# Kernel optimization log

Hardware: AMD Instinct MI355X
Metric: run time of the kernel (lower is better)

The kernel has to match this reference:

```python
import jax, jax.numpy as jnp
import numpy as np

BATCH, T, D_MODEL, D_STATE = 32, 4096, 256, 256
RMIN, RMAX, MAX_PHASE = 0.9, 0.999, 6.283
NEG_SLOPE = 0.01  # F.leaky_relu default


def setup_inputs() -> dict:
    key = jax.random.key(0)
    ks = jax.random.split(key, 12)
    x = jax.random.normal(ks[0], (BATCH, T, D_MODEL), jnp.float32)
    done = jnp.zeros((BATCH, T), jnp.bool_)
    h0_re = jnp.zeros((BATCH, D_STATE), jnp.float32)
    h0_im = jnp.zeros((BATCH, D_STATE), jnp.float32)
    # LRU eigenvalue init: |lambda| ~ U[rmin, rmax] (Orvieto et al.)
    u1 = jax.random.uniform(ks[1], (D_STATE,), jnp.float32)
    u2 = jax.random.uniform(ks[2], (D_STATE,), jnp.float32)
    nu_log = jnp.log(-0.5 * jnp.log(u1 * (RMAX**2 - RMIN**2) + RMIN**2))
    theta_log = jnp.log(MAX_PHASE * u2)
    lam_abs = jnp.exp(-jnp.exp(nu_log))
    gamma_log = jnp.log(jnp.sqrt(1.0 - lam_abs**2))
    sB = 1.0 / np.sqrt(2.0 * D_MODEL)
    sC = 1.0 / np.sqrt(D_STATE)
    B_re = jax.random.normal(ks[3], (D_STATE, D_MODEL), jnp.float32) * sB
    B_im = jax.random.normal(ks[4], (D_STATE, D_MODEL), jnp.float32) * sB
    C_re = jax.random.normal(ks[5], (D_STATE, D_STATE), jnp.float32) * sC
    C_im = jax.random.normal(ks[6], (D_STATE, D_STATE), jnp.float32) * sC
    D_mat = jax.random.normal(ks[7], (D_STATE, D_MODEL), jnp.float32) * (1.0 / np.sqrt(D_MODEL))
    mlp_w = jax.random.normal(ks[8], (D_MODEL, D_STATE), jnp.float32) * (1.0 / np.sqrt(D_STATE))
    mlp_b = jnp.zeros((D_MODEL,), jnp.float32)
    ln1_g = jnp.ones((D_MODEL,), jnp.float32); ln1_b = jnp.zeros((D_MODEL,), jnp.float32)
    ln2_g = jnp.ones((D_STATE,), jnp.float32); ln2_b = jnp.zeros((D_STATE,), jnp.float32)
    ln3_g = jnp.ones((D_MODEL,), jnp.float32); ln3_b = jnp.zeros((D_MODEL,), jnp.float32)
    return dict(x=x, done=done, h0_re=h0_re, h0_im=h0_im, nu_log=nu_log,
                theta_log=theta_log, gamma_log=gamma_log, B_re=B_re, B_im=B_im,
                C_re=C_re, C_im=C_im, D_mat=D_mat, mlp_w=mlp_w, mlp_b=mlp_b,
                ln1_g=ln1_g, ln1_b=ln1_b, ln2_g=ln2_g, ln2_b=ln2_b,
                ln3_g=ln3_g, ln3_b=ln3_b)


def _layernorm(x, g, b, eps=1e-5):
    mu = jnp.mean(x, axis=-1, keepdims=True)
    var = jnp.var(x, axis=-1, keepdims=True)
    return (x - mu) * jax.lax.rsqrt(var + eps) * g + b


def _leaky(x):
    return jnp.where(x >= 0, x, NEG_SLOPE * x)


def _forward(x, done, h0_re, h0_im, nu_log, theta_log, gamma_log, B_re, B_im,
             C_re, C_im, D_mat, mlp_w, mlp_b, ln1_g, ln1_b, ln2_g, ln2_b,
             ln3_g, ln3_b):
    z = _layernorm(x, ln1_g, ln1_b)          # [B,T,D]
    skip = z
    z = _leaky(z)
    # diagonal complex recurrence params
    lam_abs = jnp.exp(-jnp.exp(nu_log))
    theta = jnp.exp(theta_log)
    lam_re = lam_abs * jnp.cos(theta)        # [N]
    lam_im = lam_abs * jnp.sin(theta)
    gamma = jnp.exp(gamma_log)
    # input projection: gamma * (B z_t), complex
    u_re = jnp.einsum('btd,nd->btn', z, B_re) * gamma
    u_im = jnp.einsum('btd,nd->btn', z, B_im) * gamma
    mask = 1.0 - done.astype(z.dtype)        # [B,T], reset state where done

    def step(carry, inp):
        hr, hi = carry
        ur, ui, m = inp                       # [B,N],[B,N],[B]
        hr = hr * m[:, None]
        hi = hi * m[:, None]
        nr = lam_re * hr - lam_im * hi + ur
        ni = lam_re * hi + lam_im * hr + ui
        return (nr, ni), (nr, ni)

    xs = (jnp.swapaxes(u_re, 0, 1), jnp.swapaxes(u_im, 0, 1), jnp.swapaxes(mask, 0, 1))
    (_, _), (hs_re, hs_im) = jax.lax.scan(step, (h0_re, h0_im), xs)
    hs_re = jnp.swapaxes(hs_re, 0, 1)         # [B,T,N]
    hs_im = jnp.swapaxes(hs_im, 0, 1)
    # y = Re(C h) + D z
    y = (jnp.einsum('btn,mn->btm', hs_re, C_re)
         - jnp.einsum('btn,mn->btm', hs_im, C_im)
         + jnp.einsum('btd,nd->btn', z, D_mat))
    y = _leaky(_layernorm(y, ln2_g, ln2_b))
    y = jnp.einsum('btn,dn->btd', y, mlp_w) + mlp_b
    y = _layernorm(y, ln3_g, ln3_b)
    return y + skip


def reference(x, done, h0_re, h0_im, nu_log, theta_log, gamma_log, B_re, B_im,
              C_re, C_im, D_mat, mlp_w, mlp_b, ln1_g, ln1_b, ln2_g, ln2_b,
              ln3_g, ln3_b):
    return _forward(x, done, h0_re, h0_im, nu_log, theta_log, gamma_log,
                    B_re, B_im, C_re, C_im, D_mat, mlp_w, mlp_b,
                    ln1_g, ln1_b, ln2_g, ln2_b, ln3_g, ln3_b)
```

## Files before the change

kernel.cpp:

```cpp
#include <hip/hip_runtime.h>

#define BATCH 32
#define TLEN  4096
#define DM    256
#define NS    256
#define BT    (BATCH*TLEN)
#define CHL   64
#define NCH   (TLEN/CHL)

typedef unsigned short u16;
typedef __bf16 bf16x8 __attribute__((ext_vector_type(8)));
typedef float  f32x4  __attribute__((ext_vector_type(4)));

__device__ __forceinline__ u16 f2bf(float f) {
  unsigned u = __builtin_bit_cast(unsigned, f);
  u += 0x7FFFu + ((u >> 16) & 1u);
  return (u16)(u >> 16);
}
__device__ __forceinline__ float bf2f(u16 h) {
  unsigned u = ((unsigned)h) << 16;
  return __builtin_bit_cast(float, u);
}
__device__ __forceinline__ float wsum(float v) {
  #pragma unroll
  for (int m = 32; m >= 1; m >>= 1) v += __shfl_xor(v, m, 64);
  return v;
}
__device__ __forceinline__ void gload_lds16(const void* g, void* l) {
  __builtin_amdgcn_global_load_lds(
      (const __attribute__((address_space(1))) void*)(uintptr_t)g,
      (__attribute__((address_space(3))) void*)(unsigned)(uintptr_t)l,
      16, 0, 0);
}
#define VMCNT(N)  asm volatile("s_waitcnt vmcnt(" #N ")" ::: "memory")
#define LGKM0()   asm volatile("s_waitcnt lgkmcnt(0)" ::: "memory")
#define BARRIER() do { __builtin_amdgcn_s_barrier(); asm volatile("" ::: "memory"); } while (0)

__global__ void k_prep(const float* __restrict__ nu_log, const float* __restrict__ th_log,
                       const float* __restrict__ ga_log,
                       const float* __restrict__ B_re, const float* __restrict__ B_im,
                       const float* __restrict__ C_re, const float* __restrict__ C_im,
                       const float* __restrict__ D_mat, const float* __restrict__ mlp_w,
                       float* __restrict__ lam_re, float* __restrict__ lam_im,
                       u16* __restrict__ WB, u16* __restrict__ W2, u16* __restrict__ WM)
{
  const int tid = blockIdx.x * blockDim.x + threadIdx.x;
  const int nt  = gridDim.x * blockDim.x;
  for (int i = tid; i < NS; i += nt) {
    float la = expf(-expf(nu_log[i]));
    float th = expf(th_log[i]);
    lam_re[i] = la * cosf(th);
    lam_im[i] = la * sinf(th);
  }
  for (int i = tid; i < 512 * DM; i += nt) {
    int n = i >> 8, d = i & 255;
    float v = (n < 256) ? B_re[n * DM + d] * expf(ga_log[n])
                        : B_im[(n - 256) * DM + d] * expf(ga_log[n - 256]);
    WB[i] = f2bf(v);
  }
  for (int i = tid; i < 256 * 768; i += nt) {
    int n = i / 768, k = i - n * 768;
    float v;
    if (k < 256)      v =  C_re[n * 256 + k];
    else if (k < 512) v = -C_im[n * 256 + (k - 256)];
    else              v =  D_mat[n * 256 + (k - 512)];
    W2[i] = f2bf(v);
  }
  for (int i = tid; i < 256 * 256; i += nt) WM[i] = f2bf(mlp_w[i]);
}

__global__ __launch_bounds__(256) void k_ln1(const float* __restrict__ x,
                                             const float* __restrict__ g, const float* __restrict__ b,
                                             u16* __restrict__ zskip, u16* __restrict__ za)
{
  const size_t row = (size_t)blockIdx.x * 4 + (threadIdx.x >> 6);
  const int lane = threadIdx.x & 63;
  float4 v = ((const float4*)(x + row * DM))[lane];
  float s = wsum(v.x + v.y + v.z + v.w);
  float q = wsum(v.x * v.x + v.y * v.y + v.z * v.z + v.w * v.w);
  float mean = s * (1.f / DM);
  float rstd = rsqrtf(q * (1.f / DM) - mean * mean + 1e-5f);
  float4 gg = ((const float4*)g)[lane];
  float4 bb = ((const float4*)b)[lane];
  float z0 = (v.x - mean) * rstd * gg.x + bb.x;
  float z1 = (v.y - mean) * rstd * gg.y + bb.y;
  float z2 = (v.z - mean) * rstd * gg.z + bb.z;
  float z3 = (v.w - mean) * rstd * gg.w + bb.w;
  ushort4 zs, zl;
  zs.x = f2bf(z0); zs.y = f2bf(z1); zs.z = f2bf(z2); zs.w = f2bf(z3);
  zl.x = f2bf(z0 >= 0.f ? z0 : 0.01f * z0);
  zl.y = f2bf(z1 >= 0.f ? z1 : 0.01f * z1);
  zl.z = f2bf(z2 >= 0.f ? z2 : 0.01f * z2);
  zl.w = f2bf(z3 >= 0.f ? z3 : 0.01f * z3);
  ((ushort4*)(zskip + row * DM))[lane] = zs;
  ((ushort4*)(za    + row * DM))[lane] = zl;
}

template <int EPI>
__global__ __launch_bounds__(512, 2) void gemm_fused(
    const u16* __restrict__ A0, int lda0, int ksplit,
    const u16* __restrict__ A1, int lda1,
    int K, const u16* __restrict__ W, int ldw,
    const float* __restrict__ g, const float* __restrict__ b,
    const float* __restrict__ bias, const u16* __restrict__ zskip,
    u16* __restrict__ outb, float* __restrict__ outf, int ldo)
{
  __shared__ __align__(16) u16 As[2][256 * 64];
  __shared__ __align__(16) u16 Bs[2][256 * 64];
  const int m0 = blockIdx.x * 256;
  const int nw0 = blockIdx.y << 8;
  const int tid = threadIdx.x;
  const int w = tid >> 6, lane = tid & 63;
  const int wr = w >> 1, wc = w & 1;

  f32x4 acc[4][8] = {};

  auto STAGE_A = [&](int p, int k0, int half) {
    const bool second = (k0 >= ksplit);
    const u16* Asrc = second ? A1 : A0;
    const int  alda = second ? lda1 : lda0;
    const int  ak   = second ? (k0 - ksplit) : k0;
    #pragma unroll
    for (int j = 0; j < 2; ++j) {
      const int r = half * 16 + w * 2 + j;
      const int row = r * 8 + (lane >> 3);
      const int col = (((lane & 7) ^ (row & 7)) << 3);
      gload_lds16(Asrc + (size_t)(m0 + row) * alda + ak + col, &As[p][r * 512]);
    }
  };
  auto STAGE_B = [&](int p, int k0, int half) {
    #pragma unroll
    for (int j = 0; j < 2; ++j) {
      const int r = half * 16 + w * 2 + j;
      const int row = r * 8 + (lane >> 3);
      const int col = (((lane & 7) ^ (row & 7)) << 3);
      gload_lds16(W + (size_t)(nw0 + row) * ldw + k0 + col, &Bs[p][r * 512]);
    }
  };

  const int NT = K >> 6;
  STAGE_A(0, 0, 0); STAGE_A(0, 0, 1);
  STAGE_B(0, 0, 0); STAGE_B(0, 0, 1);
  if (NT > 1) { STAGE_A(1, 64, 0); STAGE_A(1, 64, 1); VMCNT(4); }
  else        { VMCNT(0); }
  BARRIER();

  const int lq = (lane >> 4) << 3;

  for (int t = 0; t < NT; ++t) {
    const int p = t & 1;
    const int pn = p ^ 1;
    bf16x8 af[4][2];
    bf16x8 bfr[2][2];

    #pragma unroll
    for (int mi = 0; mi < 4; ++mi) {
      const int ra = wr * 64 + mi * 16 + (lane & 15);
      #pragma unroll
      for (int kki = 0; kki < 2; ++kki) {
        const int koff = kki * 32 + lq;
        af[mi][kki] = *(const bf16x8*)((const char*)&As[p][0] + ra * 128 + ((koff * 2) ^ ((ra & 7) << 4)));
      }
    }
    #pragma unroll
    for (int nn = 0; nn < 2; ++nn) {
      const int rb = wc * 128 + nn * 16 + (lane & 15);
      #pragma unroll
      for (int kki = 0; kki < 2; ++kki) {
        const int koff = kki * 32 + lq;
        bfr[nn][kki] = *(const bf16x8*)((const char*)&Bs[p][0] + rb * 128 + ((koff * 2) ^ ((rb & 7) << 4)));
      }
    }
    if (t + 1 < NT) STAGE_B(pn, (t + 1) << 6, 0);
    BARRIER(); LGKM0();
    __builtin_amdgcn_s_setprio(1);
    #pragma unroll
    for (int kki = 0; kki < 2; ++kki)
      #pragma unroll
      for (int nn = 0; nn < 2; ++nn)
        #pragma unroll
        for (int mi = 0; mi < 4; ++mi)
          acc[mi][nn] = __builtin_amdgcn_mfma_f32_16x16x32_bf16(af[mi][kki], bfr[nn][kki], acc[mi][nn], 0, 0, 0);
    __builtin_amdgcn_s_setprio(0);
    BARRIER();

    #pragma unroll
    for (int q = 1; q < 4; ++q) {
      #pragma unroll
      for (int nn = 0; nn < 2; ++nn) {
        const int rb = wc * 128 + (q * 2 + nn) * 16 + (lane & 15);
        #pragma unroll
        for (int kki = 0; kki < 2; ++kki) {
          const int koff = kki * 32 + lq;
          bfr[nn][kki] = *(const bf16x8*)((const char*)&Bs[p][0] + rb * 128 + ((koff * 2) ^ ((rb & 7) << 4)));
        }
      }
      if (q == 1)      { if (t + 1 < NT) STAGE_B(pn, (t + 1) << 6, 1); }
      else if (q == 2) { if (t + 2 < NT) STAGE_A(p,  (t + 2) << 6, 0); }
      else             { if (t + 2 < NT) STAGE_A(p,  (t + 2) << 6, 1); }
      BARRIER(); LGKM0();
      __builtin_amdgcn_s_setprio(1);
      #pragma unroll
      for (int kki = 0; kki < 2; ++kki)
        #pragma unroll
        for (int nn = 0; nn < 2; ++nn)
          #pragma unroll
          for (int mi = 0; mi < 4; ++mi)
            acc[mi][q * 2 + nn] = __builtin_amdgcn_mfma_f32_16x16x32_bf16(af[mi][kki], bfr[nn][kki], acc[mi][q * 2 + nn], 0, 0, 0);
      __builtin_amdgcn_s_setprio(0);
      if (q == 3) { if (t + 2 < NT) { VMCNT(4); } else { VMCNT(0); } }
      BARRIER();
    }
  }

  const int rq = (lane >> 4) << 2;

  if constexpr (EPI == 0) {
    #pragma unroll
    for (int mi = 0; mi < 4; ++mi) {
      #pragma unroll
      for (int rr = 0; rr < 4; ++rr) {
        const int row = wr * 64 + mi * 16 + rq + rr;
        const size_t rbase = (size_t)(m0 + row) * ldo + nw0;
        #pragma unroll
        for (int ni = 0; ni < 8; ++ni) {
          const int col = wc * 128 + ni * 16 + (lane & 15);
          outb[rbase + col] = f2bf(acc[mi][ni][rr]);
        }
      }
    }
    return;
  }

  float g8[8], b8[8], bias8[8];
  #pragma unroll
  for (int ni = 0; ni < 8; ++ni) {
    const int col = wc * 128 + ni * 16 + (lane & 15);
    g8[ni] = g[col]; b8[ni] = b[col];
    if constexpr (EPI == 2) bias8[ni] = bias[col];
  }

  float* red = (float*)&As[0][0];
  #pragma unroll
  for (int mi = 0; mi < 4; ++mi) {
    #pragma unroll
    for (int rr = 0; rr < 4; ++rr) {
      float s = 0.f, q = 0.f;
      #pragma unroll
      for (int ni = 0; ni < 8; ++ni) {
        float v = acc[mi][ni][rr];
        if constexpr (EPI == 2) v += bias8[ni];
        s += v; q += v * v;
      }
      #pragma unroll
      for (int mm = 1; mm < 16; mm <<= 1) {
        s += __shfl_xor(s, mm, 64);
        q += __shfl_xor(q, mm, 64);
      }
      if ((lane & 15) == 0) {
        const int row = wr * 64 + mi * 16 + rq + rr;
        red[row * 4 + wc * 2]     = s;
        red[row * 4 + wc * 2 + 1] = q;
      }
    }
  }
  __syncthreads();

  #pragma unroll
  for (int mi = 0; mi < 4; ++mi) {
    #pragma unroll
    for (int rr = 0; rr < 4; ++rr) {
      const int row = wr * 64 + mi * 16 + rq + rr;
      const float S = red[row * 4] + red[row * 4 + 2];
      const float Q = red[row * 4 + 1] + red[row * 4 + 3];
      const float mean = S * (1.f / 256.f);
      const float rstd = rsqrtf(Q * (1.f / 256.f) - mean * mean + 1e-5f);
      const size_t rbase = (size_t)(m0 + row) * 256;
      #pragma unroll
      for (int ni = 0; ni < 8; ++ni) {
        const int col = wc * 128 + ni * 16 + (lane & 15);
        float v = acc[mi][ni][rr];
        if constexpr (EPI == 2) v += bias8[ni];
        float t = (v - mean) * rstd * g8[ni] + b8[ni];
        if constexpr (EPI == 1) {
          t = t >= 0.f ? t : 0.01f * t;
          outb[rbase + col] = f2bf(t);
        } else {
          outf[rbase + col] = t + bf2f(zskip[rbase + col]);
        }
      }
    }
  }
}

__global__ __launch_bounds__(256) void scan_passA(const u16* __restrict__ u,
    const unsigned char* __restrict__ done,
    const float* __restrict__ lam_re, const float* __restrict__ lam_im,
    float* __restrict__ Ere, float* __restrict__ Eim,
    float* __restrict__ Are, float* __restrict__ Aim)
{
  const int b = blockIdx.x / NCH, c = blockIdx.x % NCH;
  const int n = threadIdx.x;
  const float lr = lam_re[n], li = lam_im[n];
  float hre = 0.f, him = 0.f, pm = 1.f;
  const int t0 = c * CHL;
  for (int t = t0; t < t0 + CHL; ++t) {
    const float m = done[b * TLEN + t] ? 0.f : 1.f;
    pm *= m;
    const float hr = hre * m, hi = him * m;
    const size_t base = ((size_t)(b * TLEN + t)) * 512;
    const float ur = bf2f(u[base + n]), ui = bf2f(u[base + 256 + n]);
    hre = lr * hr - li * hi + ur;
    him = lr * hi + li * hr + ui;
  }
  const size_t idx = ((size_t)(b * NCH + c)) * NS + n;
  Ere[idx] = hre; Eim[idx] = him;
  float pr = lr, pi = li;
  #pragma unroll
  for (int s = 0; s < 6; ++s) { float a = pr * pr - pi * pi; float bq = 2.f * pr * pi; pr = a; pi = bq; }
  Are[idx] = pr * pm; Aim[idx] = pi * pm;
}

__global__ __launch_bounds__(256) void scan_comb(const float* __restrict__ h0re,
    const float* __restrict__ h0im,
    const float* __restrict__ Are, const float* __restrict__ Aim,
    const float* __restrict__ Ere, const float* __restrict__ Eim,
    float* __restrict__ Sre, float* __restrict__ Sim)
{
  const int b = blockIdx.x, n = threadIdx.x;
  float sre = h0re[b * NS + n], sim = h0im[b * NS + n];
  for (int c = 0; c < NCH; ++c) {
    const size_t idx = ((size_t)(b * NCH + c)) * NS + n;
    Sre[idx] = sre; Sim[idx] = sim;
    const float ar = Are[idx], ai = Aim[idx];
    const float nr = ar * sre - ai * sim + Ere[idx];
    const float ni = ar * sim + ai * sre + Eim[idx];
    sre = nr; sim = ni;
  }
}

__global__ __launch_bounds__(256) void scan_passC(u16* __restrict__ u,
    const unsigned char* __restrict__ done,
    const float* __restrict__ lam_re, const float* __restrict__ lam_im,
    const float* __restrict__ Sre, const float* __restrict__ Sim)
{
  const int b = blockIdx.x / NCH, c = blockIdx.x % NCH;
  const int n = threadIdx.x;
  const float lr = lam_re[n], li = lam_im[n];
  const size_t sidx = ((size_t)(b * NCH + c)) * NS + n;
  float hre = Sre[sidx], him = Sim[sidx];
  const int t0 = c * CHL;
  for (int t = t0; t < t0 + CHL; ++t) {
    const float m = done[b * TLEN + t] ? 0.f : 1.f;
    const float hr = hre * m, hi = him * m;
    const size_t base = ((size_t)(b * TLEN + t)) * 512;
    const float ur = bf2f(u[base + n]), ui = bf2f(u[base + 256 + n]);
    hre = lr * hr - li * hi + ur;
    him = lr * hi + li * hr + ui;
    u[base + n]       = f2bf(hre);
    u[base + 256 + n] = f2bf(him);
  }
}

extern "C" void kernel_launch(void* const* d_in, const int* in_sizes, int n_in,
                              void* d_out, int out_size, void* d_ws, size_t ws_size,
                              hipStream_t stream)
{
  const float* x      = (const float*)d_in[0];
  const unsigned char* done = (const unsigned char*)d_in[1];
  const float* h0re   = (const float*)d_in[2];
  const float* h0im   = (const float*)d_in[3];
  const float* nu_log = (const float*)d_in[4];
  const float* th_log = (const float*)d_in[5];
  const float* ga_log = (const float*)d_in[6];
  const float* B_re   = (const float*)d_in[7];
  const float* B_im   = (const float*)d_in[8];
  const float* C_re   = (const float*)d_in[9];
  const float* C_im   = (const float*)d_in[10];
  const float* D_mat  = (const float*)d_in[11];
  const float* mlp_w  = (const float*)d_in[12];
  const float* mlp_b  = (const float*)d_in[13];
  const float* ln1_g  = (const float*)d_in[14];
  const float* ln1_b  = (const float*)d_in[15];
  const float* ln2_g  = (const float*)d_in[16];
  const float* ln2_b  = (const float*)d_in[17];
  const float* ln3_g  = (const float*)d_in[18];
  const float* ln3_b  = (const float*)d_in[19];
  (void)in_sizes; (void)n_in; (void)out_size; (void)ws_size;

  char* ws = (char*)d_ws;
  float* lam_re = (float*)(ws + 0);
  float* lam_im = (float*)(ws + 1024);
  u16* WB = (u16*)(ws + 4096);
  u16* W2 = (u16*)(ws + 4096 + 512 * 256 * 2);
  u16* WM = (u16*)(ws + 4096 + 512 * 256 * 2 + 256 * 768 * 2);

  size_t off = (size_t)1 << 20;
  u16* zskip = (u16*)(ws + off); off += (size_t)BT * DM * 2;
  u16* za    = (u16*)(ws + off); off += (size_t)BT * DM * 2;
  u16* ubuf  = (u16*)(ws + off); off += (size_t)BT * 512 * 2;
  u16* ybuf  = (u16*)(ws + off); off += (size_t)BT * NS * 2;
  float* Ere = (float*)(ws + off); off += (size_t)BATCH * NCH * NS * 4;
  float* Eim = (float*)(ws + off); off += (size_t)BATCH * NCH * NS * 4;
  float* Are = (float*)(ws + off); off += (size_t)BATCH * NCH * NS * 4;
  float* Aim = (float*)(ws + off); off += (size_t)BATCH * NCH * NS * 4;
  float* Sre = (float*)(ws + off); off += (size_t)BATCH * NCH * NS * 4;
  float* Sim = (float*)(ws + off); off += (size_t)BATCH * NCH * NS * 4;

  k_prep<<<256, 256, 0, stream>>>(nu_log, th_log, ga_log, B_re, B_im, C_re, C_im,
                                  D_mat, mlp_w, lam_re, lam_im, WB, W2, WM);
  k_ln1<<<BT / 4, 256, 0, stream>>>(x, ln1_g, ln1_b, zskip, za);
  gemm_fused<0><<<dim3(BT / 256, 2), 512, 0, stream>>>(za, 256, 1 << 28, nullptr, 0,
                                                       256, WB, 256, nullptr, nullptr,
                                                       nullptr, nullptr, ubuf, nullptr, 512);
  scan_passA<<<BATCH * NCH, 256, 0, stream>>>(ubuf, done, lam_re, lam_im, Ere, Eim, Are, Aim);
  scan_comb <<<BATCH,       256, 0, stream>>>(h0re, h0im, Are, Aim, Ere, Eim, Sre, Sim);
  scan_passC<<<BATCH * NCH, 256, 0, stream>>>(ubuf, done, lam_re, lam_im, Sre, Sim);
  gemm_fused<1><<<dim3(BT / 256, 1), 512, 0, stream>>>(ubuf, 512, 512, za, 256,
                                                       768, W2, 768, ln2_g, ln2_b,
                                                       nullptr, nullptr, ybuf, nullptr, 256);
  gemm_fused<2><<<dim3(BT / 256, 1), 512, 0, stream>>>(ybuf, 256, 256, ybuf, 256,
                                                       256, WM, 256, ln3_g, ln3_b,
                                                       mlp_b, zskip, nullptr, (float*)d_out, 256);
}
```

Measured before the change: 349.6 us.

## Fuse LN2 GEMM and MLP GEMM with LN3 into one megakernel

Merges the second GEMM (with LN2+leaky epilogue) and the MLP GEMM (with LN3 and skip add) into a single kernel. The intermediate activation stays in shared memory as bf16 instead of being written to and re-read from a global ybuf. The first GEMM is also specialized with compile-time K and strides. The second GEMM reads the MLP weights straight from global memory without LDS staging, which may stall on memory latency, and the extra accumulator registers may hurt occupancy.

```diff
diff --git a/kernel.cpp b/kernel.cpp
--- a/kernel.cpp
+++ b/kernel.cpp
@@ -96,14 +96,9 @@
   ((ushort4*)(za    + row * DM))[lane] = zl;
 }
 
-template <int EPI>
-__global__ __launch_bounds__(512, 2) void gemm_fused(
-    const u16* __restrict__ A0, int lda0, int ksplit,
-    const u16* __restrict__ A1, int lda1,
-    int K, const u16* __restrict__ W, int ldw,
-    const float* __restrict__ g, const float* __restrict__ b,
-    const float* __restrict__ bias, const u16* __restrict__ zskip,
-    u16* __restrict__ outb, float* __restrict__ outf, int ldo)
+__global__ __launch_bounds__(512, 2) void gemm_u4(
+    const u16* __restrict__ A0, const u16* __restrict__ W,
+    u16* __restrict__ outb)
 {
   __shared__ __align__(16) u16 As[2][256 * 64];
   __shared__ __align__(16) u16 Bs[2][256 * 64];
@@ -116,16 +111,12 @@
   f32x4 acc[4][8] = {};
 
   auto STAGE_A = [&](int p, int k0, int half) {
-    const bool second = (k0 >= ksplit);
-    const u16* Asrc = second ? A1 : A0;
-    const int  alda = second ? lda1 : lda0;
-    const int  ak   = second ? (k0 - ksplit) : k0;
     #pragma unroll
     for (int j = 0; j < 2; ++j) {
       const int r = half * 16 + w * 2 + j;
       const int row = r * 8 + (lane >> 3);
       const int col = (((lane & 7) ^ (row & 7)) << 3);
-      gload_lds16(Asrc + (size_t)(m0 + row) * alda + ak + col, &As[p][r * 512]);
+      gload_lds16(A0 + (size_t)(m0 + row) * 256 + k0 + col, &As[p][r * 512]);
     }
   };
   auto STAGE_B = [&](int p, int k0, int half) {
@@ -134,15 +125,14 @@
       const int r = half * 16 + w * 2 + j;
       const int row = r * 8 + (lane >> 3);
       const int col = (((lane & 7) ^ (row & 7)) << 3);
-      gload_lds16(W + (size_t)(nw0 + row) * ldw + k0 + col, &Bs[p][r * 512]);
+      gload_lds16(W + (size_t)(nw0 + row) * 256 + k0 + col, &Bs[p][r * 512]);
     }
   };
 
-  const int NT = K >> 6;
+  const int NT = 4;
   STAGE_A(0, 0, 0); STAGE_A(0, 0, 1);
   STAGE_B(0, 0, 0); STAGE_B(0, 0, 1);
-  if (NT > 1) { STAGE_A(1, 64, 0); STAGE_A(1, 64, 1); VMCNT(4); }
-  else        { VMCNT(0); }
+  STAGE_A(1, 64, 0); STAGE_A(1, 64, 1); VMCNT(4);
   BARRIER();
 
   const int lq = (lane >> 4) << 3;
@@ -214,44 +204,152 @@
   }
 
   const int rq = (lane >> 4) << 2;
-
-  if constexpr (EPI == 0) {
+  #pragma unroll
+  for (int mi = 0; mi < 4; ++mi) {
+    #pragma unroll
+    for (int rr = 0; rr < 4; ++rr) {
+      const int row = wr * 64 + mi * 16 + rq + rr;
+      const size_t rbase = (size_t)(m0 + row) * 512 + nw0;
+      #pragma unroll
+      for (int ni = 0; ni < 8; ++ni) {
+        const int col = wc * 128 + ni * 16 + (lane & 15);
+        outb[rbase + col] = f2bf(acc[mi][ni][rr]);
+      }
+    }
+  }
+}
+
+__global__ __launch_bounds__(512, 2) void gemm_mega(
+    const u16* __restrict__ A0, int lda0, int ksplit,
+    const u16* __restrict__ A1, int lda1,
+    int K, const u16* __restrict__ W, int ldw,
+    const float* __restrict__ g2, const float* __restrict__ b2,
+    const u16* __restrict__ WM, const float* __restrict__ mlp_b,
+    const float* __restrict__ g3, const float* __restrict__ b3,
+    const u16* __restrict__ zskip, float* __restrict__ outf)
+{
+  __shared__ __align__(16) u16 SH[4 * 256 * 64];
+  const int m0 = blockIdx.x * 256;
+  const int tid = threadIdx.x;
+  const int w = tid >> 6, lane = tid & 63;
+  const int wr = w >> 1, wc = w & 1;
+
+  f32x4 acc[4][8] = {};
+
+  auto STAGE_A = [&](int p, int k0, int half) {
+    const bool second = (k0 >= ksplit);
+    const u16* Asrc = second ? A1 : A0;
+    const int  alda = second ? lda1 : lda0;
+    const int  ak   = second ? (k0 - ksplit) : k0;
+    #pragma unroll
+    for (int j = 0; j < 2; ++j) {
+      const int r = half * 16 + w * 2 + j;
+      const int row = r * 8 + (lane >> 3);
+      const int col = (((lane & 7) ^ (row & 7)) << 3);
+      gload_lds16(Asrc + (size_t)(m0 + row) * alda + ak + col, SH + p * 16384 + r * 512);
+    }
+  };
+  auto STAGE_B = [&](int p, int k0, int half) {
+    #pragma unroll
+    for (int j = 0; j < 2; ++j) {
+      const int r = half * 16 + w * 2 + j;
+      const int row = r * 8 + (lane >> 3);
+      const int col = (((lane & 7) ^ (row & 7)) << 3);
+      gload_lds16(W + (size_t)row * ldw + k0 + col, SH + 32768 + p * 16384 + r * 512);
+    }
+  };
+
+  const int NT = K >> 6;
+  STAGE_A(0, 0, 0); STAGE_A(0, 0, 1);
+  STAGE_B(0, 0, 0); STAGE_B(0, 0, 1);
+  STAGE_A(1, 64, 0); STAGE_A(1, 64, 1); VMCNT(4);
+  BARRIER();
+
+  const int lq = (lane >> 4) << 3;
+
+  for (int t = 0; t < NT; ++t) {
+    const int p = t & 1;
+    const int pn = p ^ 1;
+    const u16* Ab = SH + p * 16384;
+    const u16* Bb = SH + 32768 + p * 16384;
+    bf16x8 af[4][2];
+    bf16x8 bfr[2][2];
+
     #pragma unroll
     for (int mi = 0; mi < 4; ++mi) {
-      #pragma unroll
-      for (int rr = 0; rr < 4; ++rr) {
-        const int row = wr * 64 + mi * 16 + rq + rr;
-        const size_t rbase = (size_t)(m0 + row) * ldo + nw0;
+      const int ra = wr * 64 + mi * 16 + (lane & 15);
+      #pragma unroll
+      for (int kki = 0; kki < 2; ++kki) {
+        const int koff = kki * 32 + lq;
+        af[mi][kki] = *(const bf16x8*)((const char*)Ab + ra * 128 + ((koff * 2) ^ ((ra & 7) << 4)));
+      }
+    }
+    #pragma unroll
+    for (int nn = 0; nn < 2; ++nn) {
+      const int rb = wc * 128 + nn * 16 + (lane & 15);
+      #pragma unroll
+      for (int kki = 0; kki < 2; ++kki) {
+        const int koff = kki * 32 + lq;
+        bfr[nn][kki] = *(const bf16x8*)((const char*)Bb + rb * 128 + ((koff * 2) ^ ((rb & 7) << 4)));
+      }
+    }
+    if (t + 1 < NT) STAGE_B(pn, (t + 1) << 6, 0);
+    BARRIER(); LGKM0();
+    __builtin_amdgcn_s_setprio(1);
+    #pragma unroll
+    for (int kki = 0; kki < 2; ++kki)
+      #pragma unroll
+      for (int nn = 0; nn < 2; ++nn)
         #pragma unroll
-        for (int ni = 0; ni < 8; ++ni) {
-          const int col = wc * 128 + ni * 16 + (lane & 15);
-          outb[rbase + col] = f2bf(acc[mi][ni][rr]);
+        for (int mi = 0; mi < 4; ++mi)
+          acc[mi][nn] = __builtin_amdgcn_mfma_f32_16x16x32_bf16(af[mi][kki], bfr[nn][kki], acc[mi][nn], 0, 0, 0);
+    __builtin_amdgcn_s_setprio(0);
+    BARRIER();
+
+    #pragma unroll
+    for (int q = 1; q < 4; ++q) {
+      #pragma unroll
+      for (int nn = 0; nn < 2; ++nn) {
+        const int rb = wc * 128 + (q * 2 + nn) * 16 + (lane & 15);
+        #pragma unroll
+        for (int kki = 0; kki < 2; ++kki) {
+          const int koff = kki * 32 + lq;
+          bfr[nn][kki] = *(const bf16x8*)((const char*)Bb + rb * 128 + ((koff * 2) ^ ((rb & 7) << 4)));
         }
       }
-    }
-    return;
-  }
-
-  float g8[8], b8[8], bias8[8];
+      if (q == 1)      { if (t + 1 < NT) STAGE_B(pn, (t + 1) << 6, 1); }
+      else if (q == 2) { if (t + 2 < NT) STAGE_A(p,  (t + 2) << 6, 0); }
+      else             { if (t + 2 < NT) STAGE_A(p,  (t + 2) << 6, 1); }
+      BARRIER(); LGKM0();
+      __builtin_amdgcn_s_setprio(1);
+      #pragma unroll
+      for (int kki = 0; kki < 2; ++kki)
+        #pragma unroll
+        for (int nn = 0; nn < 2; ++nn)
+          #pragma unroll
+          for (int mi = 0; mi < 4; ++mi)
+            acc[mi][q * 2 + nn] = __builtin_amdgcn_mfma_f32_16x16x32_bf16(af[mi][kki], bfr[nn][kki], acc[mi][q * 2 + nn], 0, 0, 0);
+      __builtin_amdgcn_s_setprio(0);
+      if (q == 3) { if (t + 2 < NT) { VMCNT(4); } else { VMCNT(0); } }
+      BARRIER();
+    }
+  }
+
+  const int rq = (lane >> 4) << 2;
+  float g8[8], b8[8];
   #pragma unroll
   for (int ni = 0; ni < 8; ++ni) {
     const int col = wc * 128 + ni * 16 + (lane & 15);
-    g8[ni] = g[col]; b8[ni] = b[col];
-    if constexpr (EPI == 2) bias8[ni] = bias[col];
-  }
-
-  float* red = (float*)&As[0][0];
+    g8[ni] = g2[col]; b8[ni] = b2[col];
+  }
+  float* red = (float*)SH;
   #pragma unroll
   for (int mi = 0; mi < 4; ++mi) {
     #pragma unroll
     for (int rr = 0; rr < 4; ++rr) {
       float s = 0.f, q = 0.f;
       #pragma unroll
-      for (int ni = 0; ni < 8; ++ni) {
-        float v = acc[mi][ni][rr];
-        if constexpr (EPI == 2) v += bias8[ni];
-        s += v; q += v * v;
-      }
+      for (int ni = 0; ni < 8; ++ni) { float v = acc[mi][ni][rr]; s += v; q += v * v; }
       #pragma unroll
       for (int mm = 1; mm < 16; mm <<= 1) {
         s += __shfl_xor(s, mm, 64);
@@ -265,29 +363,102 @@
     }
   }
   __syncthreads();
-
+  float mean2[4][4], rstd2[4][4];
   #pragma unroll
   for (int mi = 0; mi < 4; ++mi) {
     #pragma unroll
     for (int rr = 0; rr < 4; ++rr) {
       const int row = wr * 64 + mi * 16 + rq + rr;
-      const float S = red[row * 4] + red[row * 4 + 2];
-      const float Q = red[row * 4 + 1] + red[row * 4 + 3];
+      const f32x4 rv = *(const f32x4*)(red + row * 4);
+      const float S = rv[0] + rv[2], Q = rv[1] + rv[3];
+      mean2[mi][rr] = S * (1.f / 256.f);
+      rstd2[mi][rr] = rsqrtf(Q * (1.f / 256.f) - mean2[mi][rr] * mean2[mi][rr] + 1e-5f);
+    }
+  }
+  __syncthreads();
+  #pragma unroll
+  for (int mi = 0; mi < 4; ++mi) {
+    #pragma unroll
+    for (int rr = 0; rr < 4; ++rr) {
+      const int row = wr * 64 + mi * 16 + rq + rr;
+      #pragma unroll
+      for (int ni = 0; ni < 8; ++ni) {
+        const int col = wc * 128 + ni * 16 + (lane & 15);
+        float t = (acc[mi][ni][rr] - mean2[mi][rr]) * rstd2[mi][rr] * g8[ni] + b8[ni];
+        t = t >= 0.f ? t : 0.01f * t;
+        SH[row * 256 + (col ^ ((row & 7) << 3))] = f2bf(t);
+      }
+    }
+  }
+  __syncthreads();
+
+  f32x4 acc2[4][8] = {};
+  #pragma unroll
+  for (int s = 0; s < 8; ++s) {
+    const int k = s * 32 + lq;
+    bf16x8 af2[4], bf2[8];
+    #pragma unroll
+    for (int mi = 0; mi < 4; ++mi) {
+      const int row = wr * 64 + mi * 16 + (lane & 15);
+      af2[mi] = *(const bf16x8*)&SH[row * 256 + (k ^ ((row & 7) << 3))];
+    }
+    #pragma unroll
+    for (int ni = 0; ni < 8; ++ni) {
+      const int col = wc * 128 + ni * 16 + (lane & 15);
+      bf2[ni] = *(const bf16x8*)(WM + (size_t)col * 256 + k);
+    }
+    #pragma unroll
+    for (int ni = 0; ni < 8; ++ni)
+      #pragma unroll
+      for (int mi = 0; mi < 4; ++mi)
+        acc2[mi][ni] = __builtin_amdgcn_mfma_f32_16x16x32_bf16(af2[mi], bf2[ni], acc2[mi][ni], 0, 0, 0);
+  }
+  __syncthreads();
+
+  float bias8[8], g38[8], b38[8];
+  #pragma unroll
+  for (int ni = 0; ni < 8; ++ni) {
+    const int col = wc * 128 + ni * 16 + (lane & 15);
+    bias8[ni] = mlp_b[col]; g38[ni] = g3[col]; b38[ni] = b3[col];
+  }
+  #pragma unroll
+  for (int mi = 0; mi < 4; ++mi) {
+    #pragma unroll
+    for (int rr = 0; rr < 4; ++rr) {
+      float s = 0.f, q = 0.f;
+      #pragma unroll
+      for (int ni = 0; ni < 8; ++ni) {
+        float v = acc2[mi][ni][rr] + bias8[ni];
+        s += v; q += v * v;
+      }
+      #pragma unroll
+      for (int mm = 1; mm < 16; mm <<= 1) {
+        s += __shfl_xor(s, mm, 64);
+        q += __shfl_xor(q, mm, 64);
+      }
+      if ((lane & 15) == 0) {
+        const int row = wr * 64 + mi * 16 + rq + rr;
+        red[row * 4 + wc * 2]     = s;
+        red[row * 4 + wc * 2 + 1] = q;
+      }
+    }
+  }
+  __syncthreads();
+  #pragma unroll
+  for (int mi = 0; mi < 4; ++mi) {
+    #pragma unroll
+    for (int rr = 0; rr < 4; ++rr) {
+      const int row = wr * 64 + mi * 16 + rq + rr;
+      const f32x4 rv = *(const f32x4*)(red + row * 4);
+      const float S = rv[0] + rv[2], Q = rv[1] + rv[3];
       const float mean = S * (1.f / 256.f);
       const float rstd = rsqrtf(Q * (1.f / 256.f) - mean * mean + 1e-5f);
       const size_t rbase = (size_t)(m0 + row) * 256;
       #pragma unroll
       for (int ni = 0; ni < 8; ++ni) {
         const int col = wc * 128 + ni * 16 + (lane & 15);
-        float v = acc[mi][ni][rr];
-        if constexpr (EPI == 2) v += bias8[ni];
-        float t = (v - mean) * rstd * g8[ni] + b8[ni];
-        if constexpr (EPI == 1) {
-          t = t >= 0.f ? t : 0.01f * t;
-          outb[rbase + col] = f2bf(t);
-        } else {
-          outf[rbase + col] = t + bf2f(zskip[rbase + col]);
-        }
+        const float v = acc2[mi][ni][rr] + bias8[ni];
+        outf[rbase + col] = (v - mean) * rstd * g38[ni] + b38[ni] + bf2f(zskip[rbase + col]);
       }
     }
   }
@@ -399,7 +570,6 @@
   u16* zskip = (u16*)(ws + off); off += (size_t)BT * DM * 2;
   u16* za    = (u16*)(ws + off); off += (size_t)BT * DM * 2;
   u16* ubuf  = (u16*)(ws + off); off += (size_t)BT * 512 * 2;
-  u16* ybuf  = (u16*)(ws + off); off += (size_t)BT * NS * 2;
   float* Ere = (float*)(ws + off); off += (size_t)BATCH * NCH * NS * 4;
   float* Eim = (float*)(ws + off); off += (size_t)BATCH * NCH * NS * 4;
   float* Are = (float*)(ws + off); off += (size_t)BATCH * NCH * NS * 4;
@@ -410,16 +580,12 @@
   k_prep<<<256, 256, 0, stream>>>(nu_log, th_log, ga_log, B_re, B_im, C_re, C_im,
                                   D_mat, mlp_w, lam_re, lam_im, WB, W2, WM);
   k_ln1<<<BT / 4, 256, 0, stream>>>(x, ln1_g, ln1_b, zskip, za);
-  gemm_fused<0><<<dim3(BT / 256, 2), 512, 0, stream>>>(za, 256, 1 << 28, nullptr, 0,
-                                                       256, WB, 256, nullptr, nullptr,
-                                                       nullptr, nullptr, ubuf, nullptr, 512);
+  gemm_u4<<<dim3(BT / 256, 2), 512, 0, stream>>>(za, WB, ubuf);
   scan_passA<<<BATCH * NCH, 256, 0, stream>>>(ubuf, done, lam_re, lam_im, Ere, Eim, Are, Aim);
   scan_comb <<<BATCH,       256, 0, stream>>>(h0re, h0im, Are, Aim, Ere, Eim, Sre, Sim);
   scan_passC<<<BATCH * NCH, 256, 0, stream>>>(ubuf, done, lam_re, lam_im, Sre, Sim);
-  gemm_fused<1><<<dim3(BT / 256, 1), 512, 0, stream>>>(ubuf, 512, 512, za, 256,
-                                                       768, W2, 768, ln2_g, ln2_b,
-                                                       nullptr, nullptr, ybuf, nullptr, 256);
-  gemm_fused<2><<<dim3(BT / 256, 1), 512, 0, stream>>>(ybuf, 256, 256, ybuf, 256,
-                                                       256, WM, 256, ln3_g, ln3_b,
-                                                       mlp_b, zskip, nullptr, (float*)d_out, 256);
-}
+  gemm_mega<<<BT / 256, 512, 0, stream>>>(ubuf, 512, 512, za, 256,
+                                          768, W2, 768, ln2_g, ln2_b,
+                                          WM, mlp_b, ln3_g, ln3_b,
+                                          zskip, (float*)d_out);
+}
```

After: 368.2 us. +5.3%, slower.
